# Kernel tuning notes

Measured on AMD Instinct MI355X. Metric: run time of the kernel, lower is better.

The kernel has to match this reference:

```python
import jax, jax.numpy as jnp
import numpy as np

IN_CH, HID, OUT_CH = 1, 16, 1

def _conv(x, w, b, pad):
    # x: [B,C,H,W], w: [O,I,kh,kw], b: [O]
    y = jax.lax.conv_general_dilated(
        x, w, window_strides=(1, 1), padding=[(pad, pad), (pad, pad)],
        dimension_numbers=('NCHW', 'OIHW', 'NCHW'))
    return y + b[None, :, None, None]

def setup_inputs() -> dict:
    key = jax.random.key(0)
    ks = jax.random.split(key, 8)
    def w_init(k, shape):
        fan_in = shape[1] * shape[2] * shape[3]
        return jax.random.normal(k, shape, dtype=jnp.float32) * (1.0 / np.sqrt(fan_in))
    B, H, W = 32, 256, 256
    return {
        'x': jax.random.normal(ks[0], (B, IN_CH, H, W), dtype=jnp.float32),
        'w_perceive': w_init(ks[1], (HID * 2, IN_CH + HID, 3, 3)),
        'b_perceive': jnp.zeros((HID * 2,), jnp.float32),
        'w_up1': w_init(ks[2], (HID, HID * 2, 1, 1)),
        'b_up1': jnp.zeros((HID,), jnp.float32),
        'w_up2': w_init(ks[3], (HID, HID, 1, 1)),
        'b_up2': jnp.zeros((HID,), jnp.float32),
        'w_tau': w_init(ks[4], (HID, IN_CH + HID * 2, 3, 3)),
        'b_tau_conv': jnp.zeros((HID,), jnp.float32),
        'b_tau': jnp.ones((1, HID, 1, 1), jnp.float32) * 1.5,
        'w_read': w_init(ks[5], (OUT_CH, HID, 1, 1)),
        'b_read': jnp.zeros((OUT_CH,), jnp.float32),
        'n_steps': 10,
    }

def reference(x, w_perceive, b_perceive, w_up1, b_up1, w_up2, b_up2,
              w_tau, b_tau_conv, b_tau, w_read, b_read, n_steps):
    B, _, H, W = x.shape
    state = jnp.zeros((B, HID, H, W), dtype=x.dtype)

    def step(state, _):
        combined = jnp.concatenate([x, state], axis=1)          # [B, in+hid, H, W]
        perception = _conv(combined, w_perceive, b_perceive, 1)  # [B, 2*hid, H, W]
        h1 = jax.nn.relu(_conv(perception, w_up1, b_up1, 0))
        delta = _conv(h1, w_up2, b_up2, 0)                       # [B, hid, H, W]
        tau_input = jnp.concatenate([x, state, delta], axis=1)  # [B, in+2*hid, H, W]
        tau_logit = _conv(tau_input, w_tau, b_tau_conv, 1) + b_tau
        beta = jnp.clip(jax.nn.sigmoid(tau_logit), 0.01, 0.99)
        return beta * state + (1.0 - beta) * delta, None

    state, _ = jax.lax.scan(step, state, None, length=n_steps)
    return jax.nn.sigmoid(_conv(state, w_read, b_read, 0))
```

## Files before the change

### kernel.cpp

```cpp
#include <hip/hip_runtime.h>
#include <hip/hip_bf16.h>
#include <math.h>


#define B_   32
#define H_   256
#define W_   256
#define PIT  40
#define XPP  260

typedef unsigned short ushort_t;
typedef __attribute__((ext_vector_type(8))) short short8;
typedef __attribute__((ext_vector_type(4))) float float4v;

__device__ __forceinline__ unsigned fbits(float f) {
    union { float f; unsigned u; } v; v.f = f; return v.u;
}
__device__ __forceinline__ ushort_t f2bu(float f) {
    return (ushort_t)((fbits(f) + 0x8000u) >> 16);
}
__device__ __forceinline__ unsigned pack2(float lo, float hi) {
    return ((fbits(hi) + 0x8000u) & 0xFFFF0000u) | ((fbits(lo) + 0x8000u) >> 16);
}
__device__ __forceinline__ float bu2f(ushort_t u) {
    union { unsigned i; float f; } v; v.i = ((unsigned)u) << 16; return v.f;
}
__device__ __forceinline__ float lo2f(unsigned u) {
    union { unsigned i; float f; } v; v.i = u << 16; return v.f;
}
__device__ __forceinline__ float hi2f(unsigned u) {
    union { unsigned i; float f; } v; v.i = u & 0xFFFF0000u; return v.f;
}

__global__ void prep(
    const float* __restrict__ wp,
    const float* __restrict__ wu1,
    const float* __restrict__ bu1,
    const float* __restrict__ bp,
    const float* __restrict__ wu2,
    const float* __restrict__ wt,
    const float* __restrict__ btc,
    const float* __restrict__ bt,
    ushort_t* __restrict__ wh1p,
    ushort_t* __restrict__ wu2f,
    ushort_t* __restrict__ wtxf,
    ushort_t* __restrict__ wtn,
    float* __restrict__ scal)
{
    __shared__ float Weff[16 * 153];
    const int tid = threadIdx.x;

    for (int i = tid; i < 16 * 153; i += 256) {
        int j = i / 153, rem = i % 153, c = rem / 9, t = rem % 9;
        float s = 0.f;
        for (int o = 0; o < 32; ++o)
            s += wu1[j * 32 + o] * wp[o * 153 + c * 9 + t];
        Weff[i] = s;
    }
    if (tid < 16) {
        float s = bu1[tid];
        for (int o = 0; o < 32; ++o) s += wu1[tid * 32 + o] * bp[o];
        scal[tid] = s;
    }
    if (tid < 16) scal[32 + tid] = btc[tid] + bt[tid];
    if (tid < 16) scal[48 + tid] = wt[tid * 297 + 8];
    __syncthreads();

    if (tid < 16) scal[16 + tid] = Weff[tid * 153 + 8];

    for (int i = tid; i < 4 * 64 * 8; i += 256) {
        int ii = i >> 9, lane = (i >> 3) & 63, j = i & 7;
        int n = lane & 15, kk = ((lane >> 4) << 3) + j;
        int tap = 2 * ii + (kk >> 4), ch = kk & 15;
        wh1p[i] = f2bu(Weff[n * 153 + (ch + 1) * 9 + tap]);
    }
    for (int i = tid; i < 512; i += 256) {
        int lane = i >> 3, j = i & 7;
        int n = lane & 15, k = ((lane >> 4) << 3) + j;
        float v = 0.f;
        if (k < 16)      v = Weff[n * 153 + (k + 1) * 9 + 8];
        else if (k < 24) v = Weff[n * 153 + (k - 16)];
        wh1p[2048 + i] = f2bu(v);
    }
    for (int i = tid; i < 512; i += 256) {
        int lane = i >> 3, j = i & 7;
        int n = lane & 15, k = ((lane >> 4) << 3) + j;
        wu2f[i] = (k < 16) ? f2bu(wu2[n * 16 + k]) : (ushort_t)0;
    }
    for (int i = tid; i < 512; i += 256) {
        int lane = i >> 3, j = i & 7;
        int n = lane & 15, k = ((lane >> 4) << 3) + j;
        wtxf[i] = (k < 8) ? f2bu(wt[n * 297 + k]) : (ushort_t)0;
    }
    for (int i = tid; i < 9 * 64 * 8; i += 256) {
        int t = i / 512, lane = (i / 8) % 64, j = i % 8;
        int n = lane & 15, k = ((lane >> 4) << 3) + j;
        int c = (k < 16) ? (17 + k) : (k - 15);
        wtn[i] = f2bu(wt[n * 297 + c * 9 + t]);
    }
}

__global__ __launch_bounds__(256) void precompute_xp8(
    const float* __restrict__ x,
    ushort_t* __restrict__ xp8)
{
    int idx = blockIdx.x * 256 + threadIdx.x;
    if (idx >= B_ * XPP * XPP) return;
    int b  = idx / (XPP * XPP), rem = idx - b * (XPP * XPP);
    int by = rem / XPP, bx = rem - by * XPP;
    int gy = by - 2, gx = bx - 2;
    const float* xb = x + (size_t)b * 65536;
    short8 v;
#pragma unroll
    for (int t = 0; t < 8; ++t) {
        int yy = gy + t / 3, xx = gx + t % 3;
        bool in = ((unsigned)yy < 256u) & ((unsigned)xx < 256u);
        v[t] = in ? (short)f2bu(xb[yy * 256 + xx]) : (short)0;
    }
    *(short8*)(xp8 + (size_t)idx * 8) = v;
}

__global__ __launch_bounds__(256) void nca_step(
    const ushort_t* __restrict__ stIn,
    ushort_t* __restrict__ stOut,
    const ushort_t* __restrict__ xp8g,
    const ushort_t* __restrict__ wh1p,
    const ushort_t* __restrict__ wu2f,
    const ushort_t* __restrict__ wtxf,
    const ushort_t* __restrict__ wtn,
    const float* __restrict__ scal,
    const float* __restrict__ bu2G,
    const float* __restrict__ wrd,
    const float* __restrict__ brd,
    float* __restrict__ outg,
    int first, int last)
{
    __shared__ ushort_t comb[400 * PIT];

    const int tid  = threadIdx.x;
    const int w    = tid >> 6, lane = tid & 63;
    const int m    = lane & 15, q = lane >> 4;
    const int och  = q * 4;
    const int gx0  = blockIdx.x * 16, gy0 = blockIdx.y * 16;
    const size_t pb = (size_t)blockIdx.z * 65536;
    const size_t xpb = (size_t)blockIdx.z * (XPP * XPP);
    const short8 z8 = {0, 0, 0, 0, 0, 0, 0, 0};
    const float4v z4 = {0.f, 0.f, 0.f, 0.f};

    short8 wh1r[5], wtnr[9];
#pragma unroll
    for (int i = 0; i < 5; ++i) wh1r[i] = *(const short8*)(wh1p + (i * 64 + lane) * 8);
#pragma unroll
    for (int t = 0; t < 9; ++t) wtnr[t] = *(const short8*)(wtn + (t * 64 + lane) * 8);
    const short8 wu2r = *(const short8*)(wu2f + lane * 8);
    const short8 wtxr = *(const short8*)(wtxf + lane * 8);

    float4v beff4, wxh84, bu24, wr4, tb4, wtx84;
#pragma unroll
    for (int r = 0; r < 4; ++r) {
        beff4[r] = scal[och + r];
        wxh84[r] = scal[16 + och + r];
        tb4[r]   = scal[32 + och + r];
        wtx84[r] = scal[48 + och + r];
        bu24[r]  = bu2G[och + r];
        wr4[r]   = wrd[och + r];
    }
    const float br = brd[0];

    const int sel = q >> 1;
    int offp[4];
#pragma unroll
    for (int ii = 0; ii < 4; ++ii) {
        int tA = 2 * ii, tB = 2 * ii + 1;
        int oA = ((tA / 3) * 20 + (tA % 3)) * PIT;
        int oB = ((tB / 3) * 20 + (tB % 3)) * PIT;
        offp[ii] = sel ? oB : oA;
    }
    const int chOff = 16 + (q & 1) * 8;
    const int t8off = (2 * 20 + 2) * PIT;
    const int off5  = (q == 0) ? (t8off + 16) : (q == 1) ? (t8off + 24)
                    : (q == 2) ? 32 : 16;

    const int bpA = ((m + (q << 5)) & 63) << 2;
    const bool hiq = q >= 2;

    for (int p = tid; p < 400; p += 256) {
        int ry = p / 20, rx = p - ry * 20;
        int gy = gy0 + ry - 2, gx = gx0 + rx - 2;
        ushort_t* row = comb + p * PIT;
        bool in = ((unsigned)gy < 256u) & ((unsigned)gx < 256u);
        if (in && !first) {
            const ushort_t* sp = stIn + (pb + gy * 256 + gx) * 16;
            *(short8*)(row + 16) = *(const short8*)(sp);
            *(short8*)(row + 24) = *(const short8*)(sp + 8);
        } else {
            *(short8*)(row + 16) = z8; *(short8*)(row + 24) = z8;
        }
        *(short8*)(row + 32) = *(const short8*)(
            xp8g + (xpb + (size_t)(gy0 + ry) * XPP + (gx0 + rx)) * 8);
    }
    __syncthreads();

    for (int i = 0; i < 6; ++i) {
        int g = w + 4 * i; if (g >= 21) break;
        int raw = g * 16 + m;
        int idx = (raw > 323) ? 323 : raw;
        int py = idx / 18, px = idx - py * 18;
        const ushort_t* abase = comb + (py * 20 + px) * PIT;
        float4v acc = z4;
#pragma unroll
        for (int ii = 0; ii < 4; ++ii) {
            short8 b = *(const short8*)(abase + offp[ii] + chOff);
            acc = __builtin_amdgcn_mfma_f32_16x16x32_bf16(wh1r[ii], b, acc, 0, 0, 0);
        }
        {
            short8 b = *(const short8*)(abase + off5);
            acc = __builtin_amdgcn_mfma_f32_16x16x32_bf16(wh1r[4], b, acc, 0, 0, 0);
        }
        float x8 = bu2f(comb[((py + 2) * 20 + px + 2) * PIT + 32]);
        uint2 hv;
        {
            float h0 = fmaxf(acc[0] + beff4[0] + x8 * wxh84[0], 0.f);
            float h1 = fmaxf(acc[1] + beff4[1] + x8 * wxh84[1], 0.f);
            float h2 = fmaxf(acc[2] + beff4[2] + x8 * wxh84[2], 0.f);
            float h3 = fmaxf(acc[3] + beff4[3] + x8 * wxh84[3], 0.f);
            hv.x = pack2(h0, h1); hv.y = pack2(h2, h3);
        }
        int vx0 = __builtin_amdgcn_ds_bpermute(bpA,      (int)hv.x);
        int vy0 = __builtin_amdgcn_ds_bpermute(bpA,      (int)hv.y);
        int vx1 = __builtin_amdgcn_ds_bpermute(bpA + 64, (int)hv.x);
        int vy1 = __builtin_amdgcn_ds_bpermute(bpA + 64, (int)hv.y);
        union { int i4[4]; short8 s8; } bb;
        bb.i4[0] = hiq ? 0 : vx0;  bb.i4[1] = hiq ? 0 : vy0;
        bb.i4[2] = hiq ? 0 : vx1;  bb.i4[3] = hiq ? 0 : vy1;
        float4v d = __builtin_amdgcn_mfma_f32_16x16x32_bf16(wu2r, bb.s8, z4, 0, 0, 0);
        bool vld = raw < 324;
        int gy = gy0 - 1 + py, gx = gx0 - 1 + px;
        bool im = vld & ((unsigned)gy < 256u) & ((unsigned)gx < 256u);
        uint2 dv;
        dv.x = pack2(d[0] + bu24[0], d[1] + bu24[1]);
        dv.y = pack2(d[2] + bu24[2], d[3] + bu24[3]);
        if (!im) { dv.x = 0u; dv.y = 0u; }
        if (vld)
            *(uint2*)(comb + ((py + 1) * 20 + (px + 1)) * PIT + och) = dv;
    }
    __syncthreads();

    for (int i = 0; i < 4; ++i) {
        int g = w * 4 + i;
        const ushort_t* cb = comb + ((g + 1) * 20 + (m + 1)) * PIT;
        float4v acc = z4;
#pragma unroll
        for (int t = 0; t < 9; ++t) {
            short8 b = *(const short8*)(cb + ((t / 3) * 20 + (t % 3)) * PIT + q * 8);
            acc = __builtin_amdgcn_mfma_f32_16x16x32_bf16(wtnr[t], b, acc, 0, 0, 0);
        }
        {
            short8 bx = *(const short8*)(cb + 32);
            acc = __builtin_amdgcn_mfma_f32_16x16x32_bf16(wtxr, bx, acc, 0, 0, 0);
        }
        int gy = gy0 + g;
        const size_t pix = pb + gy * 256 + gx0 + m;
        const ushort_t* cpx = comb + ((g + 2) * 20 + (m + 2)) * PIT;
        float x8c = bu2f(comb[((g + 3) * 20 + (m + 3)) * PIT + 32]);
        uint2 su = *(const uint2*)(cpx + 16 + och);
        uint2 du = *(const uint2*)(cpx + och);
        float sold[4] = { lo2f(su.x), hi2f(su.x), lo2f(su.y), hi2f(su.y) };
        float dvv[4]  = { lo2f(du.x), hi2f(du.x), lo2f(du.y), hi2f(du.y) };
        float sn[4];
#pragma unroll
        for (int r = 0; r < 4; ++r) {
            float tl  = acc[r] + tb4[r] + x8c * wtx84[r];
            float e   = __expf(-tl);
            float bta = __builtin_amdgcn_rcpf(1.f + e);
            bta = fminf(fmaxf(bta, 0.01f), 0.99f);
            sn[r] = dvv[r] + bta * (sold[r] - dvv[r]);
        }
        if (!last) {
            uint2 o;
            o.x = pack2(sn[0], sn[1]); o.y = pack2(sn[2], sn[3]);
            *(uint2*)(stOut + pix * 16 + och) = o;
        } else {
            float v = sn[0] * wr4[0] + sn[1] * wr4[1]
                    + sn[2] * wr4[2] + sn[3] * wr4[3];
            v += __shfl_xor(v, 16);
            v += __shfl_xor(v, 32);
            if (q == 0) {
                float eo = __expf(-(v + br));
                outg[pix] = __builtin_amdgcn_rcpf(1.f + eo);
            }
        }
    }
}

extern "C" void kernel_launch(void* const* d_in, const int* in_sizes, int n_in,
                              void* d_out, int out_size, void* d_ws, size_t ws_size,
                              hipStream_t stream)
{
    const float* x          = (const float*)d_in[0];
    const float* w_perceive = (const float*)d_in[1];
    const float* b_perceive = (const float*)d_in[2];
    const float* w_up1      = (const float*)d_in[3];
    const float* b_up1      = (const float*)d_in[4];
    const float* w_up2      = (const float*)d_in[5];
    const float* b_up2      = (const float*)d_in[6];
    const float* w_tau      = (const float*)d_in[7];
    const float* b_tau_conv = (const float*)d_in[8];
    const float* b_tau      = (const float*)d_in[9];
    const float* w_read     = (const float*)d_in[10];
    const float* b_read     = (const float*)d_in[11];
    float* out = (float*)d_out;

    const size_t stateElems = (size_t)B_ * H_ * W_ * 16;
    const size_t xp8Elems   = (size_t)B_ * XPP * XPP * 8;

    ushort_t* stA  = (ushort_t*)d_ws;
    ushort_t* stB  = stA + stateElems;
    ushort_t* xp8g = stB + stateElems;
    ushort_t* wh1p = xp8g + xp8Elems;
    ushort_t* wu2f = wh1p + 2560;
    ushort_t* wtxf = wu2f + 512;
    ushort_t* wtn  = wtxf + 512;
    float*    scal = (float*)(wtn + 4608);

    const size_t needBytes = (2 * stateElems + xp8Elems
                              + 2560 + 512 + 512 + 4608) * sizeof(ushort_t)
                           + 64 * sizeof(float);
    if (ws_size < needBytes) return;

    prep<<<dim3(1), dim3(256), 0, stream>>>(
        w_perceive, w_up1, b_up1, b_perceive, w_up2, w_tau,
        b_tau_conv, b_tau, wh1p, wu2f, wtxf, wtn, scal);
    precompute_xp8<<<dim3((B_ * XPP * XPP + 255) / 256), dim3(256), 0, stream>>>(
        x, xp8g);

    ushort_t* cur = stA;
    ushort_t* nxt = stB;
    for (int s = 0; s < 10; ++s) {
        nca_step<<<dim3(16, 16, 32), dim3(256), 0, stream>>>(
            cur, nxt, xp8g, wh1p, wu2f, wtxf, wtn, scal, b_up2,
            w_read, b_read, out, (s == 0) ? 1 : 0, (s == 9) ? 1 : 0);
        ushort_t* t = cur; cur = nxt; nxt = t;
    }
}
```

Baseline: 795.3 us.

## Fold x center tap into MFMA, add interior fast path, reuse tau rows

Moves the x center-tap contribution of the perceive stage into the fifth MFMA's K slots, which removes a per-pixel LDS load and FMA. Interior tiles get a load path and a delta store without bounds checks. Pixel index math is now incremental instead of using divisions. The tau conv keeps a rolling window of three LDS rows in registers, so each row is loaded once instead of three times, and s_setprio brackets the MFMA chains. The cost is more registers and two code paths to keep consistent.

```diff
diff --git a/kernel.cpp b/kernel.cpp
--- a/kernel.cpp
+++ b/kernel.cpp
@@ -78,8 +78,9 @@
         int lane = i >> 3, j = i & 7;
         int n = lane & 15, k = ((lane >> 4) << 3) + j;
         float v = 0.f;
-        if (k < 16)      v = Weff[n * 153 + (k + 1) * 9 + 8];
-        else if (k < 24) v = Weff[n * 153 + (k - 16)];
+        if (k < 16)       v = Weff[n * 153 + (k + 1) * 9 + 8];
+        else if (k < 24)  v = Weff[n * 153 + (k - 16)];
+        else if (k == 24) v = Weff[n * 153 + 8];
         wh1p[2048 + i] = f2bu(v);
     }
     for (int i = tid; i < 512; i += 256) {
@@ -147,6 +148,9 @@
     const short8 z8 = {0, 0, 0, 0, 0, 0, 0, 0};
     const float4v z4 = {0.f, 0.f, 0.f, 0.f};
 
+    const bool interior = (blockIdx.x >= 1) & (blockIdx.x <= 14)
+                        & (blockIdx.y >= 1) & (blockIdx.y <= 14);
+
     short8 wh1r[5], wtnr[9];
 #pragma unroll
     for (int i = 0; i < 5; ++i) wh1r[i] = *(const short8*)(wh1p + (i * 64 + lane) * 8);
@@ -155,11 +159,10 @@
     const short8 wu2r = *(const short8*)(wu2f + lane * 8);
     const short8 wtxr = *(const short8*)(wtxf + lane * 8);
 
-    float4v beff4, wxh84, bu24, wr4, tb4, wtx84;
+    float4v beff4, bu24, wr4, tb4, wtx84;
 #pragma unroll
     for (int r = 0; r < 4; ++r) {
         beff4[r] = scal[och + r];
-        wxh84[r] = scal[16 + och + r];
         tb4[r]   = scal[32 + och + r];
         wtx84[r] = scal[48 + och + r];
         bu24[r]  = bu2G[och + r];
@@ -179,117 +182,151 @@
     const int chOff = 16 + (q & 1) * 8;
     const int t8off = (2 * 20 + 2) * PIT;
     const int off5  = (q == 0) ? (t8off + 16) : (q == 1) ? (t8off + 24)
-                    : (q == 2) ? 32 : 16;
+                    : (q == 2) ? 32 : (t8off + 32);
 
     const int bpA = ((m + (q << 5)) & 63) << 2;
     const bool hiq = q >= 2;
 
-    for (int p = tid; p < 400; p += 256) {
-        int ry = p / 20, rx = p - ry * 20;
-        int gy = gy0 + ry - 2, gx = gx0 + rx - 2;
-        ushort_t* row = comb + p * PIT;
-        bool in = ((unsigned)gy < 256u) & ((unsigned)gx < 256u);
-        if (in && !first) {
-            const ushort_t* sp = stIn + (pb + gy * 256 + gx) * 16;
+    if (interior & (first == 0)) {
+        for (int p = tid; p < 400; p += 256) {
+            int ry = p / 20, rx = p - ry * 20;
+            ushort_t* row = comb + p * PIT;
+            const ushort_t* sp = stIn
+                + (pb + (size_t)(gy0 + ry - 2) * 256 + (gx0 + rx - 2)) * 16;
             *(short8*)(row + 16) = *(const short8*)(sp);
             *(short8*)(row + 24) = *(const short8*)(sp + 8);
-        } else {
-            *(short8*)(row + 16) = z8; *(short8*)(row + 24) = z8;
+            *(short8*)(row + 32) = *(const short8*)(
+                xp8g + (xpb + (size_t)(gy0 + ry) * XPP + (gx0 + rx)) * 8);
         }
-        *(short8*)(row + 32) = *(const short8*)(
-            xp8g + (xpb + (size_t)(gy0 + ry) * XPP + (gx0 + rx)) * 8);
+    } else {
+        for (int p = tid; p < 400; p += 256) {
+            int ry = p / 20, rx = p - ry * 20;
+            int gy = gy0 + ry - 2, gx = gx0 + rx - 2;
+            ushort_t* row = comb + p * PIT;
+            bool in = ((unsigned)gy < 256u) & ((unsigned)gx < 256u);
+            if (in && !first) {
+                const ushort_t* sp = stIn + (pb + gy * 256 + gx) * 16;
+                *(short8*)(row + 16) = *(const short8*)(sp);
+                *(short8*)(row + 24) = *(const short8*)(sp + 8);
+            } else {
+                *(short8*)(row + 16) = z8; *(short8*)(row + 24) = z8;
+            }
+            *(short8*)(row + 32) = *(const short8*)(
+                xp8g + (xpb + (size_t)(gy0 + ry) * XPP + (gx0 + rx)) * 8);
+        }
     }
     __syncthreads();
 
-    for (int i = 0; i < 6; ++i) {
-        int g = w + 4 * i; if (g >= 21) break;
-        int raw = g * 16 + m;
-        int idx = (raw > 323) ? 323 : raw;
-        int py = idx / 18, px = idx - py * 18;
-        const ushort_t* abase = comb + (py * 20 + px) * PIT;
-        float4v acc = z4;
-#pragma unroll
-        for (int ii = 0; ii < 4; ++ii) {
-            short8 b = *(const short8*)(abase + offp[ii] + chOff);
-            acc = __builtin_amdgcn_mfma_f32_16x16x32_bf16(wh1r[ii], b, acc, 0, 0, 0);
+    {
+        int raw = w * 16 + m;
+        int py = raw / 18, px = raw - (raw / 18) * 18;
+        for (int i = 0; i < 6; ++i) {
+            int g = w + 4 * i; if (g >= 21) break;
+            bool vld = raw < 324;
+            int pyc = vld ? py : 17, pxc = vld ? px : 17;
+            const ushort_t* abase = comb + (pyc * 20 + pxc) * PIT;
+            float4v acc = z4;
+            __builtin_amdgcn_s_setprio(1);
+#pragma unroll
+            for (int ii = 0; ii < 4; ++ii) {
+                short8 b = *(const short8*)(abase + offp[ii] + chOff);
+                acc = __builtin_amdgcn_mfma_f32_16x16x32_bf16(wh1r[ii], b, acc, 0, 0, 0);
+            }
+            {
+                short8 b = *(const short8*)(abase + off5);
+                acc = __builtin_amdgcn_mfma_f32_16x16x32_bf16(wh1r[4], b, acc, 0, 0, 0);
+            }
+            __builtin_amdgcn_s_setprio(0);
+            uint2 hv;
+            {
+                float h0 = fmaxf(acc[0] + beff4[0], 0.f);
+                float h1 = fmaxf(acc[1] + beff4[1], 0.f);
+                float h2 = fmaxf(acc[2] + beff4[2], 0.f);
+                float h3 = fmaxf(acc[3] + beff4[3], 0.f);
+                hv.x = pack2(h0, h1); hv.y = pack2(h2, h3);
+            }
+            int vx0 = __builtin_amdgcn_ds_bpermute(bpA,      (int)hv.x);
+            int vy0 = __builtin_amdgcn_ds_bpermute(bpA,      (int)hv.y);
+            int vx1 = __builtin_amdgcn_ds_bpermute(bpA + 64, (int)hv.x);
+            int vy1 = __builtin_amdgcn_ds_bpermute(bpA + 64, (int)hv.y);
+            union { int i4[4]; short8 s8; } bb;
+            bb.i4[0] = hiq ? 0 : vx0;  bb.i4[1] = hiq ? 0 : vy0;
+            bb.i4[2] = hiq ? 0 : vx1;  bb.i4[3] = hiq ? 0 : vy1;
+            float4v d = __builtin_amdgcn_mfma_f32_16x16x32_bf16(wu2r, bb.s8, z4, 0, 0, 0);
+            uint2 dv;
+            dv.x = pack2(d[0] + bu24[0], d[1] + bu24[1]);
+            dv.y = pack2(d[2] + bu24[2], d[3] + bu24[3]);
+            if (!interior) {
+                int gy = gy0 - 1 + pyc, gx = gx0 - 1 + pxc;
+                bool im = ((unsigned)gy < 256u) & ((unsigned)gx < 256u);
+                if (!im) { dv.x = 0u; dv.y = 0u; }
+            }
+            if (vld)
+                *(uint2*)(comb + ((pyc + 1) * 20 + (pxc + 1)) * PIT + och) = dv;
+            raw += 64; px += 10; py += 3;
+            if (px >= 18) { px -= 18; py += 1; }
         }
-        {
-            short8 b = *(const short8*)(abase + off5);
-            acc = __builtin_amdgcn_mfma_f32_16x16x32_bf16(wh1r[4], b, acc, 0, 0, 0);
+    }
+    __syncthreads();
+
+    {
+        const int w4 = w * 4;
+#define LDROW(r, dx) (*(const short8*)(comb + (((r) * 20) + (m + 1 + (dx))) * PIT + q * 8))
+        short8 Ta0 = LDROW(w4 + 1, 0), Ta1 = LDROW(w4 + 1, 1), Ta2 = LDROW(w4 + 1, 2);
+        short8 Tb0 = LDROW(w4 + 2, 0), Tb1 = LDROW(w4 + 2, 1), Tb2 = LDROW(w4 + 2, 2);
+#pragma unroll
+        for (int i = 0; i < 4; ++i) {
+            int g = w4 + i;
+            short8 Tc0 = LDROW(g + 3, 0), Tc1 = LDROW(g + 3, 1), Tc2 = LDROW(g + 3, 2);
+            short8 bx = *(const short8*)(comb + ((g + 1) * 20 + (m + 1)) * PIT + 32);
+            float4v acc = z4;
+            __builtin_amdgcn_s_setprio(1);
+            acc = __builtin_amdgcn_mfma_f32_16x16x32_bf16(wtnr[0], Ta0, acc, 0, 0, 0);
+            acc = __builtin_amdgcn_mfma_f32_16x16x32_bf16(wtnr[1], Ta1, acc, 0, 0, 0);
+            acc = __builtin_amdgcn_mfma_f32_16x16x32_bf16(wtnr[2], Ta2, acc, 0, 0, 0);
+            acc = __builtin_amdgcn_mfma_f32_16x16x32_bf16(wtnr[3], Tb0, acc, 0, 0, 0);
+            acc = __builtin_amdgcn_mfma_f32_16x16x32_bf16(wtnr[4], Tb1, acc, 0, 0, 0);
+            acc = __builtin_amdgcn_mfma_f32_16x16x32_bf16(wtnr[5], Tb2, acc, 0, 0, 0);
+            acc = __builtin_amdgcn_mfma_f32_16x16x32_bf16(wtnr[6], Tc0, acc, 0, 0, 0);
+            acc = __builtin_amdgcn_mfma_f32_16x16x32_bf16(wtnr[7], Tc1, acc, 0, 0, 0);
+            acc = __builtin_amdgcn_mfma_f32_16x16x32_bf16(wtnr[8], Tc2, acc, 0, 0, 0);
+            acc = __builtin_amdgcn_mfma_f32_16x16x32_bf16(wtxr,   bx,  acc, 0, 0, 0);
+            __builtin_amdgcn_s_setprio(0);
+            int gy = gy0 + g;
+            const size_t pix = pb + gy * 256 + gx0 + m;
+            const ushort_t* cpx = comb + ((g + 2) * 20 + (m + 2)) * PIT;
+            float x8c = bu2f(comb[((g + 3) * 20 + (m + 3)) * PIT + 32]);
+            uint2 su = *(const uint2*)(cpx + 16 + och);
+            uint2 du = *(const uint2*)(cpx + och);
+            float sold[4] = { lo2f(su.x), hi2f(su.x), lo2f(su.y), hi2f(su.y) };
+            float dvv[4]  = { lo2f(du.x), hi2f(du.x), lo2f(du.y), hi2f(du.y) };
+            float sn[4];
+#pragma unroll
+            for (int r = 0; r < 4; ++r) {
+                float tl  = acc[r] + tb4[r] + x8c * wtx84[r];
+                float e   = __expf(-tl);
+                float bta = __builtin_amdgcn_rcpf(1.f + e);
+                bta = fminf(fmaxf(bta, 0.01f), 0.99f);
+                sn[r] = dvv[r] + bta * (sold[r] - dvv[r]);
+            }
+            if (!last) {
+                uint2 o;
+                o.x = pack2(sn[0], sn[1]); o.y = pack2(sn[2], sn[3]);
+                *(uint2*)(stOut + pix * 16 + och) = o;
+            } else {
+                float v = sn[0] * wr4[0] + sn[1] * wr4[1]
+                        + sn[2] * wr4[2] + sn[3] * wr4[3];
+                v += __shfl_xor(v, 16);
+                v += __shfl_xor(v, 32);
+                if (q == 0) {
+                    float eo = __expf(-(v + br));
+                    outg[pix] = __builtin_amdgcn_rcpf(1.f + eo);
+                }
+            }
+            Ta0 = Tb0; Ta1 = Tb1; Ta2 = Tb2;
+            Tb0 = Tc0; Tb1 = Tc1; Tb2 = Tc2;
         }
-        float x8 = bu2f(comb[((py + 2) * 20 + px + 2) * PIT + 32]);
-        uint2 hv;
-        {
-            float h0 = fmaxf(acc[0] + beff4[0] + x8 * wxh84[0], 0.f);
-            float h1 = fmaxf(acc[1] + beff4[1] + x8 * wxh84[1], 0.f);
-            float h2 = fmaxf(acc[2] + beff4[2] + x8 * wxh84[2], 0.f);
-            float h3 = fmaxf(acc[3] + beff4[3] + x8 * wxh84[3], 0.f);
-            hv.x = pack2(h0, h1); hv.y = pack2(h2, h3);
-        }
-        int vx0 = __builtin_amdgcn_ds_bpermute(bpA,      (int)hv.x);
-        int vy0 = __builtin_amdgcn_ds_bpermute(bpA,      (int)hv.y);
-        int vx1 = __builtin_amdgcn_ds_bpermute(bpA + 64, (int)hv.x);
-        int vy1 = __builtin_amdgcn_ds_bpermute(bpA + 64, (int)hv.y);
-        union { int i4[4]; short8 s8; } bb;
-        bb.i4[0] = hiq ? 0 : vx0;  bb.i4[1] = hiq ? 0 : vy0;
-        bb.i4[2] = hiq ? 0 : vx1;  bb.i4[3] = hiq ? 0 : vy1;
-        float4v d = __builtin_amdgcn_mfma_f32_16x16x32_bf16(wu2r, bb.s8, z4, 0, 0, 0);
-        bool vld = raw < 324;
-        int gy = gy0 - 1 + py, gx = gx0 - 1 + px;
-        bool im = vld & ((unsigned)gy < 256u) & ((unsigned)gx < 256u);
-        uint2 dv;
-        dv.x = pack2(d[0] + bu24[0], d[1] + bu24[1]);
-        dv.y = pack2(d[2] + bu24[2], d[3] + bu24[3]);
-        if (!im) { dv.x = 0u; dv.y = 0u; }
-        if (vld)
-            *(uint2*)(comb + ((py + 1) * 20 + (px + 1)) * PIT + och) = dv;
-    }
-    __syncthreads();
-
-    for (int i = 0; i < 4; ++i) {
-        int g = w * 4 + i;
-        const ushort_t* cb = comb + ((g + 1) * 20 + (m + 1)) * PIT;
-        float4v acc = z4;
-#pragma unroll
-        for (int t = 0; t < 9; ++t) {
-            short8 b = *(const short8*)(cb + ((t / 3) * 20 + (t % 3)) * PIT + q * 8);
-            acc = __builtin_amdgcn_mfma_f32_16x16x32_bf16(wtnr[t], b, acc, 0, 0, 0);
-        }
-        {
-            short8 bx = *(const short8*)(cb + 32);
-            acc = __builtin_amdgcn_mfma_f32_16x16x32_bf16(wtxr, bx, acc, 0, 0, 0);
-        }
-        int gy = gy0 + g;
-        const size_t pix = pb + gy * 256 + gx0 + m;
-        const ushort_t* cpx = comb + ((g + 2) * 20 + (m + 2)) * PIT;
-        float x8c = bu2f(comb[((g + 3) * 20 + (m + 3)) * PIT + 32]);
-        uint2 su = *(const uint2*)(cpx + 16 + och);
-        uint2 du = *(const uint2*)(cpx + och);
-        float sold[4] = { lo2f(su.x), hi2f(su.x), lo2f(su.y), hi2f(su.y) };
-        float dvv[4]  = { lo2f(du.x), hi2f(du.x), lo2f(du.y), hi2f(du.y) };
-        float sn[4];
-#pragma unroll
-        for (int r = 0; r < 4; ++r) {
-            float tl  = acc[r] + tb4[r] + x8c * wtx84[r];
-            float e   = __expf(-tl);
-            float bta = __builtin_amdgcn_rcpf(1.f + e);
-            bta = fminf(fmaxf(bta, 0.01f), 0.99f);
-            sn[r] = dvv[r] + bta * (sold[r] - dvv[r]);
-        }
-        if (!last) {
-            uint2 o;
-            o.x = pack2(sn[0], sn[1]); o.y = pack2(sn[2], sn[3]);
-            *(uint2*)(stOut + pix * 16 + och) = o;
-        } else {
-            float v = sn[0] * wr4[0] + sn[1] * wr4[1]
-                    + sn[2] * wr4[2] + sn[3] * wr4[3];
-            v += __shfl_xor(v, 16);
-            v += __shfl_xor(v, 32);
-            if (q == 0) {
-                float eo = __expf(-(v + br));
-                outg[pix] = __builtin_amdgcn_rcpf(1.f + eo);
-            }
-        }
+#undef LDROW
     }
 }
 
```

New measurement: 715.1 us. -10.1%, faster.
